# Kernel optimization log

Measured on AMD Instinct MI355X. Metric: run time of the kernel, lower is better.

## Reference

```python
import jax, jax.numpy as jnp
import numpy as np

EMBED_DIM = 768
NUM_HEADS = 12
HEAD_DIM = EMBED_DIM // NUM_HEADS
B, T = 2, 2048


def setup_inputs() -> dict:
    key = jax.random.key(0)
    ks = jax.random.split(key, 11)
    s = 1.0 / np.sqrt(EMBED_DIM)
    return {
        "query": jax.random.normal(ks[0], (B, T, EMBED_DIM), jnp.float32),
        "key_in": jax.random.normal(ks[1], (B, T, EMBED_DIM), jnp.float32),
        "value": jax.random.normal(ks[2], (B, T, EMBED_DIM), jnp.float32),
        "Wq": jax.random.uniform(ks[3], (EMBED_DIM, EMBED_DIM), jnp.float32, -s, s),
        "bq": jnp.zeros((EMBED_DIM,), jnp.float32),
        "Wk": jax.random.uniform(ks[4], (EMBED_DIM, EMBED_DIM), jnp.float32, -s, s),
        "bk": jnp.zeros((EMBED_DIM,), jnp.float32),
        "Wv": jax.random.uniform(ks[5], (EMBED_DIM, EMBED_DIM), jnp.float32, -s, s),
        "bv": jnp.zeros((EMBED_DIM,), jnp.float32),
        "Wo": jax.random.uniform(ks[6], (EMBED_DIM, EMBED_DIM), jnp.float32, -s, s),
        "bo": jnp.zeros((EMBED_DIM,), jnp.float32),
    }


def reference(query, key_in, value, Wq, bq, Wk, bk, Wv, bv, Wo, bo):
    b, t, _ = query.shape

    def split_heads(x):  # [B,T,E] -> [B,H,T,Dh]
        return x.reshape(b, t, NUM_HEADS, HEAD_DIM).transpose(0, 2, 1, 3)

    Q = split_heads(query @ Wq + bq)
    K = split_heads(key_in @ Wk + bk)
    V = split_heads(value @ Wv + bv)

    scores = jnp.einsum("bhqd,bhkd->bhqk", Q, K) / np.sqrt(HEAD_DIM).astype(np.float32)
    attn = jax.nn.softmax(scores, axis=-1)
    out = jnp.einsum("bhqk,bhkd->bhqd", attn, V)  # [B,H,T,Dh]
    out = out.transpose(0, 2, 1, 3).reshape(b, t, EMBED_DIM)
    return out @ Wo + bo
```

## Files before the change

kernel.cpp:

```cpp
#include <hip/hip_runtime.h>
#include <math.h>

typedef __attribute__((ext_vector_type(4))) float  floatx4;
typedef __attribute__((ext_vector_type(8))) short  short8;
typedef __attribute__((ext_vector_type(4))) short  short4v;
typedef __attribute__((ext_vector_type(8))) __bf16 bf16x8;

#define E_DIM 768
#define T_DIM 2048
#define N_B   2
#define N_H   12
#define H_D   64
#define M_TOT 4096

#define Q_SCALE 0.1803368801111204f

#if __has_builtin(__builtin_amdgcn_exp2f)
#define EXP2F(x) __builtin_amdgcn_exp2f(x)
#else
#define EXP2F(x) exp2f(x)
#endif
#if __has_builtin(__builtin_amdgcn_rcpf)
#define RCPF(x) __builtin_amdgcn_rcpf(x)
#else
#define RCPF(x) (1.0f / (x))
#endif

__device__ __forceinline__ unsigned short f32_to_bf16(float f) {
  unsigned int u = __float_as_uint(f);
  u += 0x7fffu + ((u >> 16) & 1u);
  return (unsigned short)(u >> 16);
}

__device__ __forceinline__ unsigned short f32_to_bf16_trunc(float f) {
  return (unsigned short)(__float_as_uint(f) >> 16);
}

__device__ __forceinline__ void gload_lds16(const unsigned short* g, unsigned short* l) {
  __builtin_amdgcn_global_load_lds(
      (const __attribute__((address_space(1))) unsigned int*)(const void*)g,
      (__attribute__((address_space(3))) unsigned int*)(void*)l, 16, 0, 0);
}

__global__ __launch_bounds__(256) void prep(const float* __restrict__ q,
                                            const float* __restrict__ k,
                                            const float* __restrict__ v,
                                            const float* __restrict__ W0,
                                            const float* __restrict__ W1,
                                            const float* __restrict__ W2,
                                            const float* __restrict__ W3,
                                            unsigned short* __restrict__ Xb,
                                            unsigned short* __restrict__ Wt) {
  __shared__ float tile[32][33];
  const int bx = blockIdx.x;
  if (bx < 9216) {
    const int z = bx / 3072, inner = bx % 3072;
    const float* src = (z == 0) ? q : (z == 1) ? k : v;
    size_t idx = ((size_t)inner * 256 + threadIdx.x) * 4;
    float4 val = *reinterpret_cast<const float4*>(&src[idx]);
    short4v o;
    o[0] = (short)f32_to_bf16(val.x);
    o[1] = (short)f32_to_bf16(val.y);
    o[2] = (short)f32_to_bf16(val.z);
    o[3] = (short)f32_to_bf16(val.w);
    *reinterpret_cast<short4v*>(&Xb[(size_t)z * M_TOT * E_DIM + idx]) = o;
  } else {
    const int t = bx - 9216;
    const int z = t / 576, rem = t % 576;
    const float* W = (z == 0) ? W0 : (z == 1) ? W1 : (z == 2) ? W2 : W3;
    unsigned short* dst = Wt + (size_t)z * E_DIM * E_DIM;
    int k0 = (rem / 24) * 32, n0 = (rem % 24) * 32;
    int tx = threadIdx.x & 31, ty = threadIdx.x >> 5;
    for (int i = 0; i < 4; i++)
      tile[ty + i * 8][tx] = W[(size_t)(k0 + ty + i * 8) * E_DIM + n0 + tx];
    __syncthreads();
    for (int i = 0; i < 4; i++)
      dst[(size_t)(n0 + ty + i * 8) * E_DIM + k0 + tx] = f32_to_bf16(tile[tx][ty + i * 8]);
  }
}

__global__ __launch_bounds__(256) void gemm_qkv(const unsigned short* __restrict__ Xb,
                                                const unsigned short* __restrict__ WtAll,
                                                const float* __restrict__ bq,
                                                const float* __restrict__ bk,
                                                const float* __restrict__ bv,
                                                unsigned short* __restrict__ outQKV,
                                                unsigned short* __restrict__ VTout) {
  __shared__ unsigned short As[128 * 32];
  __shared__ unsigned short Bs[128 * 32];

  const int z = blockIdx.z;
  const unsigned short* A = Xb + (size_t)z * M_TOT * E_DIM;
  const float* bias = (z == 0) ? bq : (z == 1) ? bk : bv;
  const unsigned short* W = WtAll + (size_t)z * E_DIM * E_DIM;
  unsigned short* out = outQKV + (size_t)z * M_TOT * E_DIM;
  const float scale = (z == 0) ? Q_SCALE : 1.0f;

  const int tid = threadIdx.x;
  const int lane = tid & 63, wv = tid >> 6;
  const int m15 = lane & 15, quad = lane >> 4;
  const int wm = (wv & 1) * 64, wn = (wv >> 1) * 64;
  const int m0 = blockIdx.x * 128, n0 = blockIdx.y * 128;

  floatx4 acc[4][4] = {};
  const int srow = lane >> 2, scol = (lane & 3) * 8;

  for (int k0 = 0; k0 < E_DIM; k0 += 32) {
    for (int cc = 0; cc < 2; cc++) {
      int c = wv * 2 + cc;
      gload_lds16(&A[(size_t)(m0 + c * 16 + srow) * E_DIM + k0 + scol], &As[c * 512]);
      gload_lds16(&W[(size_t)(n0 + c * 16 + srow) * E_DIM + k0 + scol], &Bs[c * 512]);
    }
    __syncthreads();
    bf16x8 af[4], bfr[4];
    for (int i = 0; i < 4; i++)
      af[i] = *reinterpret_cast<const bf16x8*>(&As[(wm + i * 16 + m15) * 32 + quad * 8]);
    for (int j = 0; j < 4; j++)
      bfr[j] = *reinterpret_cast<const bf16x8*>(&Bs[(wn + j * 16 + m15) * 32 + quad * 8]);
    for (int i = 0; i < 4; i++)
      for (int j = 0; j < 4; j++)
        acc[i][j] = __builtin_amdgcn_mfma_f32_16x16x32_bf16(af[i], bfr[j], acc[i][j], 0, 0, 0);
    __syncthreads();
  }

  if (z == 2) {
    for (int i = 0; i < 4; i++)
      for (int j = 0; j < 4; j++) {
        int gn = n0 + wn + j * 16 + m15;
        int hh = gn >> 6, d = gn & 63;
        float bso = bias[gn];
        int gm0 = m0 + wm + i * 16 + quad * 4;
        int bb2 = gm0 >> 11, t0 = gm0 & 2047;
        unsigned int d0 = ((unsigned int)f32_to_bf16(acc[i][j][1] + bso) << 16) |
                          f32_to_bf16(acc[i][j][0] + bso);
        unsigned int d1 = ((unsigned int)f32_to_bf16(acc[i][j][3] + bso) << 16) |
                          f32_to_bf16(acc[i][j][2] + bso);
        uint2 dd; dd.x = d0; dd.y = d1;
        *reinterpret_cast<uint2*>(
            &VTout[(((size_t)bb2 * N_H + hh) * H_D + d) * T_DIM + t0]) = dd;
      }
  } else {
    for (int i = 0; i < 4; i++)
      for (int j = 0; j < 4; j++) {
        int gn = n0 + wn + j * 16 + m15;
        int h = gn >> 6, d = gn & 63;
        float bso = bias[gn];
        for (int r = 0; r < 4; r++) {
          int gm = m0 + wm + i * 16 + quad * 4 + r;
          int bb = gm >> 11, tt = gm & 2047;
          float vv = (acc[i][j][r] + bso) * scale;
          out[(((size_t)bb * N_H + h) * T_DIM + tt) * H_D + d] = f32_to_bf16(vv);
        }
      }
  }
}

__global__ __launch_bounds__(256) void attn(const unsigned short* __restrict__ QKV,
                                            const unsigned short* __restrict__ VT,
                                            unsigned short* __restrict__ ctx) {
  __shared__ unsigned short Kbuf[2][2][64 * 64];
  __shared__ unsigned short strips[4][32 * 72];

  const int qb = blockIdx.x, h = blockIdx.y, bb = blockIdx.z;
  const size_t headoff = (((size_t)bb * N_H + h) * T_DIM) * H_D;
  const unsigned short* Qg = QKV + headoff;
  const unsigned short* Kg = QKV + (size_t)M_TOT * E_DIM + headoff;
  const unsigned short* VTg = VT + (((size_t)bb * N_H + h) * H_D) * T_DIM;

  const int tid = threadIdx.x, lane = tid & 63, wv = tid >> 6;
  const int m15 = lane & 15, quad = lane >> 4;
  const int qs = wv & 1, ks = wv >> 1;
  const int q0 = qb * 64 + qs * 32;

  auto stage = [&](int t0, int ping) {
#pragma unroll
    for (int i = 0; i < 4; i++) {
      int c = tid + i * 256;
      int tile = c >> 9, cc = c & 511;
      int key = cc >> 3, dc = cc & 7;
      int dcs = dc ^ (key & 7);
      gload_lds16(&Kg[((size_t)(t0 + tile) * 64 + key) * 64 + dcs * 8],
                  &Kbuf[ping][tile][cc * 8]);
    }
  };

  stage(0, 0);

  bf16x8 aq[2][2];
  for (int g = 0; g < 2; g++)
    for (int kk = 0; kk < 2; kk++)
      aq[g][kk] = __builtin_bit_cast(bf16x8, *reinterpret_cast<const short8*>(
          &Qg[(size_t)(q0 + g * 16 + m15) * 64 + kk * 32 + quad * 8]));

  const unsigned short* vbase = VTg + (size_t)(m15 * 2048 + quad * 8);
#define VFRAG(kt, nt, kk2) \
  (*reinterpret_cast<const short8*>(vbase + (size_t)(nt) * 32768 + (kt) * 64 + (kk2) * 32))

  short8 vf[8];
#pragma unroll
  for (int nt = 0; nt < 4; nt++)
    for (int kk2 = 0; kk2 < 2; kk2++) vf[nt * 2 + kk2] = VFRAG(ks, nt, kk2);

  floatx4 o[2][4] = {};
  floatx4 lacc[2] = {};
  const short8 ones_s = {0x3f80, 0x3f80, 0x3f80, 0x3f80, 0x3f80, 0x3f80, 0x3f80, 0x3f80};
  const bf16x8 onesb = __builtin_bit_cast(bf16x8, ones_s);
  unsigned short* strip = strips[wv];

  for (int r = 0; r < 16; r++) {
    __syncthreads();
    if (r < 15) stage(2 * r + 2, (r + 1) & 1);
    const unsigned short* Kt = Kbuf[r & 1][ks];
    const int kt = 2 * r + ks;

    floatx4 s[2][4] = {};
    for (int kk = 0; kk < 2; kk++)
#pragma unroll
      for (int mt = 0; mt < 4; mt++) {
        bf16x8 a = *reinterpret_cast<const bf16x8*>(
            &Kt[(mt * 16 + m15) * 64 + (((kk * 4 + quad) ^ (m15 & 7)) * 8)]);
        s[0][mt] = __builtin_amdgcn_mfma_f32_16x16x32_bf16(a, aq[0][kk], s[0][mt], 0, 0, 0);
        s[1][mt] = __builtin_amdgcn_mfma_f32_16x16x32_bf16(a, aq[1][kk], s[1][mt], 0, 0, 0);
      }

    for (int g = 0; g < 2; g++)
#pragma unroll
      for (int mt = 0; mt < 4; mt++) {
        unsigned int d0 = ((unsigned int)f32_to_bf16_trunc(EXP2F(s[g][mt][1])) << 16) |
                          f32_to_bf16_trunc(EXP2F(s[g][mt][0]));
        unsigned int d1 = ((unsigned int)f32_to_bf16_trunc(EXP2F(s[g][mt][3])) << 16) |
                          f32_to_bf16_trunc(EXP2F(s[g][mt][2]));
        uint2 dd; dd.x = d0; dd.y = d1;
        *reinterpret_cast<uint2*>(&strip[(g * 16 + m15) * 72 + mt * 16 + quad * 4]) = dd;
      }
    asm volatile("s_waitcnt lgkmcnt(0)" ::: "memory");

    for (int kk2 = 0; kk2 < 2; kk2++)
      for (int g = 0; g < 2; g++) {
        bf16x8 a = *reinterpret_cast<const bf16x8*>(
            &strip[(g * 16 + m15) * 72 + kk2 * 32 + quad * 8]);
        lacc[g] = __builtin_amdgcn_mfma_f32_16x16x32_bf16(a, onesb, lacc[g], 0, 0, 0);
#pragma unroll
        for (int nt = 0; nt < 4; nt++)
          o[g][nt] = __builtin_amdgcn_mfma_f32_16x16x32_bf16(
              a, __builtin_bit_cast(bf16x8, vf[nt * 2 + kk2]), o[g][nt], 0, 0, 0);
      }

    if (r < 15)
#pragma unroll
      for (int nt = 0; nt < 4; nt++)
        for (int kk2 = 0; kk2 < 2; kk2++) vf[nt * 2 + kk2] = VFRAG(kt + 2, nt, kk2);
  }
#undef VFRAG

  __syncthreads();
  float* red = (float*)&Kbuf[0][0][0];
  if (ks == 1) {
    floatx4* dst = (floatx4*)(red + (size_t)(qs * 64 + lane) * 40);
#pragma unroll
    for (int g = 0; g < 2; g++)
      for (int nt = 0; nt < 4; nt++) dst[g * 4 + nt] = o[g][nt];
    dst[8] = lacc[0];
    dst[9] = lacc[1];
  }
  __syncthreads();
  if (ks == 0) {
    const floatx4* src = (const floatx4*)(red + (size_t)(qs * 64 + lane) * 40);
#pragma unroll
    for (int g = 0; g < 2; g++)
      for (int nt = 0; nt < 4; nt++) o[g][nt] += src[g * 4 + nt];
    lacc[0] += src[8];
    lacc[1] += src[9];
    for (int g = 0; g < 2; g++)
      for (int r4 = 0; r4 < 4; r4++) {
        float rl = RCPF(lacc[g][r4]);
        int qq = q0 + g * 16 + quad * 4 + r4;
        for (int nt = 0; nt < 4; nt++)
          ctx[(size_t)(bb * T_DIM + qq) * E_DIM + h * 64 + nt * 16 + m15] =
              f32_to_bf16(o[g][nt][r4] * rl);
      }
  }
}

__global__ __launch_bounds__(256) void gemm_out(const unsigned short* __restrict__ Actx,
                                                const unsigned short* __restrict__ Wt,
                                                const float* __restrict__ bias,
                                                float* __restrict__ out) {
  __shared__ unsigned short As[64 * 32];
  __shared__ unsigned short Bs[128 * 32];

  const int tid = threadIdx.x;
  const int lane = tid & 63, wv = tid >> 6;
  const int m15 = lane & 15, quad = lane >> 4;
  const int wm = (wv & 1) * 32, wn = (wv >> 1) * 64;
  const int m0 = blockIdx.x * 64, n0 = blockIdx.y * 128;

  floatx4 acc[2][4] = {};
  const int srow = lane >> 2, scol = (lane & 3) * 8;

  for (int k0 = 0; k0 < E_DIM; k0 += 32) {
    gload_lds16(&Actx[(size_t)(m0 + wv * 16 + srow) * E_DIM + k0 + scol], &As[wv * 512]);
    for (int cc = 0; cc < 2; cc++) {
      int c = wv * 2 + cc;
      gload_lds16(&Wt[(size_t)(n0 + c * 16 + srow) * E_DIM + k0 + scol], &Bs[c * 512]);
    }
    __syncthreads();
    bf16x8 af[2], bfr[4];
    for (int i = 0; i < 2; i++)
      af[i] = *reinterpret_cast<const bf16x8*>(&As[(wm + i * 16 + m15) * 32 + quad * 8]);
    for (int j = 0; j < 4; j++)
      bfr[j] = *reinterpret_cast<const bf16x8*>(&Bs[(wn + j * 16 + m15) * 32 + quad * 8]);
    for (int i = 0; i < 2; i++)
      for (int j = 0; j < 4; j++)
        acc[i][j] = __builtin_amdgcn_mfma_f32_16x16x32_bf16(af[i], bfr[j], acc[i][j], 0, 0, 0);
    __syncthreads();
  }

  for (int i = 0; i < 2; i++)
    for (int j = 0; j < 4; j++) {
      int gn = n0 + wn + j * 16 + m15;
      float bso = bias[gn];
      for (int r = 0; r < 4; r++) {
        int gm = m0 + wm + i * 16 + quad * 4 + r;
        out[(size_t)gm * E_DIM + gn] = acc[i][j][r] + bso;
      }
    }
}

extern "C" void kernel_launch(void* const* d_in, const int* in_sizes, int n_in,
                              void* d_out, int out_size, void* d_ws, size_t ws_size,
                              hipStream_t stream) {
  const float* query  = (const float*)d_in[0];
  const float* key_in = (const float*)d_in[1];
  const float* value  = (const float*)d_in[2];
  const float* Wq = (const float*)d_in[3];
  const float* bq = (const float*)d_in[4];
  const float* Wk = (const float*)d_in[5];
  const float* bk = (const float*)d_in[6];
  const float* Wv = (const float*)d_in[7];
  const float* bv = (const float*)d_in[8];
  const float* Wo = (const float*)d_in[9];
  const float* bo = (const float*)d_in[10];
  float* out = (float*)d_out;

  unsigned short* ws  = (unsigned short*)d_ws;
  unsigned short* Wt  = ws;
  unsigned short* Xb  = Wt + (size_t)4 * E_DIM * E_DIM;
  unsigned short* QKV = Xb + (size_t)3 * M_TOT * E_DIM;
  unsigned short* VT  = QKV + (size_t)3 * M_TOT * E_DIM;
  unsigned short* ctx = VT + (size_t)N_B * N_H * H_D * T_DIM;

  dim3 tb(256);
  prep<<<dim3(11520), tb, 0, stream>>>(query, key_in, value, Wq, Wk, Wv, Wo, Xb, Wt);
  gemm_qkv<<<dim3(32, 6, 3), tb, 0, stream>>>(Xb, Wt, bq, bk, bv, QKV, VT);
  attn<<<dim3(32, 12, 2), tb, 0, stream>>>(QKV, VT, ctx);
  gemm_out<<<dim3(64, 6), tb, 0, stream>>>(ctx, Wt + (size_t)3 * E_DIM * E_DIM, bo, out);
  (void)in_sizes; (void)n_in; (void)out_size; (void)ws_size;
}
```

Baseline: 213.7 us.

## Software-pipeline attention with register K fragments and double-buffered P strips

The attention kernel stops staging K tiles through shared memory with block-wide barriers. Each wave now loads its K fragments straight from global memory into registers. The loop is skewed so that the PV MFMAs for the previous tile overlap the QK and exp work for the current tile, using double-buffered per-wave P strips. Launch bounds request 3 blocks per CU. The QKV GEMM also moves to a K-step of 64 with XOR-swizzled LDS, which halves the number of barrier pairs. The trade-offs are more register pressure and uncoalesced direct global loads of K.

```diff
diff --git a/kernel.cpp b/kernel.cpp
--- a/kernel.cpp
+++ b/kernel.cpp
@@ -86,8 +86,8 @@
                                                 const float* __restrict__ bv,
                                                 unsigned short* __restrict__ outQKV,
                                                 unsigned short* __restrict__ VTout) {
-  __shared__ unsigned short As[128 * 32];
-  __shared__ unsigned short Bs[128 * 32];
+  __shared__ unsigned short As[128 * 64];
+  __shared__ unsigned short Bs[128 * 64];
 
   const int z = blockIdx.z;
   const unsigned short* A = Xb + (size_t)z * M_TOT * E_DIM;
@@ -103,23 +103,31 @@
   const int m0 = blockIdx.x * 128, n0 = blockIdx.y * 128;
 
   floatx4 acc[4][4] = {};
-  const int srow = lane >> 2, scol = (lane & 3) * 8;
-
-  for (int k0 = 0; k0 < E_DIM; k0 += 32) {
-    for (int cc = 0; cc < 2; cc++) {
-      int c = wv * 2 + cc;
-      gload_lds16(&A[(size_t)(m0 + c * 16 + srow) * E_DIM + k0 + scol], &As[c * 512]);
-      gload_lds16(&W[(size_t)(n0 + c * 16 + srow) * E_DIM + k0 + scol], &Bs[c * 512]);
-    }
-    __syncthreads();
-    bf16x8 af[4], bfr[4];
-    for (int i = 0; i < 4; i++)
-      af[i] = *reinterpret_cast<const bf16x8*>(&As[(wm + i * 16 + m15) * 32 + quad * 8]);
-    for (int j = 0; j < 4; j++)
-      bfr[j] = *reinterpret_cast<const bf16x8*>(&Bs[(wn + j * 16 + m15) * 32 + quad * 8]);
-    for (int i = 0; i < 4; i++)
+  const int sw = m15 & 7;
+
+  for (int k0 = 0; k0 < E_DIM; k0 += 64) {
+#pragma unroll
+    for (int i = 0; i < 4; i++) {
+      int c = tid + i * 256;
+      int row = c >> 3, dc = c & 7;
+      int dcs = dc ^ (row & 7);
+      gload_lds16(&A[(size_t)(m0 + row) * E_DIM + k0 + dcs * 8], &As[c * 8]);
+      gload_lds16(&W[(size_t)(n0 + row) * E_DIM + k0 + dcs * 8], &Bs[c * 8]);
+    }
+    __syncthreads();
+#pragma unroll
+    for (int kk = 0; kk < 2; kk++) {
+      bf16x8 af[4], bfr[4];
+      for (int i = 0; i < 4; i++)
+        af[i] = *reinterpret_cast<const bf16x8*>(
+            &As[(wm + i * 16 + m15) * 64 + (((kk * 4 + quad) ^ sw) * 8)]);
       for (int j = 0; j < 4; j++)
-        acc[i][j] = __builtin_amdgcn_mfma_f32_16x16x32_bf16(af[i], bfr[j], acc[i][j], 0, 0, 0);
+        bfr[j] = *reinterpret_cast<const bf16x8*>(
+            &Bs[(wn + j * 16 + m15) * 64 + (((kk * 4 + quad) ^ sw) * 8)]);
+      for (int i = 0; i < 4; i++)
+        for (int j = 0; j < 4; j++)
+          acc[i][j] = __builtin_amdgcn_mfma_f32_16x16x32_bf16(af[i], bfr[j], acc[i][j], 0, 0, 0);
+    }
     __syncthreads();
   }
 
@@ -155,11 +163,10 @@
   }
 }
 
-__global__ __launch_bounds__(256) void attn(const unsigned short* __restrict__ QKV,
-                                            const unsigned short* __restrict__ VT,
-                                            unsigned short* __restrict__ ctx) {
-  __shared__ unsigned short Kbuf[2][2][64 * 64];
-  __shared__ unsigned short strips[4][32 * 72];
+__global__ __launch_bounds__(256, 3) void attn(const unsigned short* __restrict__ QKV,
+                                               const unsigned short* __restrict__ VT,
+                                               unsigned short* __restrict__ ctx) {
+  __shared__ unsigned short strips[4][2][32 * 72];
 
   const int qb = blockIdx.x, h = blockIdx.y, bb = blockIdx.z;
   const size_t headoff = (((size_t)bb * N_H + h) * T_DIM) * H_D;
@@ -172,19 +179,12 @@
   const int qs = wv & 1, ks = wv >> 1;
   const int q0 = qb * 64 + qs * 32;
 
-  auto stage = [&](int t0, int ping) {
-#pragma unroll
-    for (int i = 0; i < 4; i++) {
-      int c = tid + i * 256;
-      int tile = c >> 9, cc = c & 511;
-      int key = cc >> 3, dc = cc & 7;
-      int dcs = dc ^ (key & 7);
-      gload_lds16(&Kg[((size_t)(t0 + tile) * 64 + key) * 64 + dcs * 8],
-                  &Kbuf[ping][tile][cc * 8]);
-    }
-  };
-
-  stage(0, 0);
+  const unsigned short* kbase = Kg + (size_t)(m15 * 64 + quad * 8);
+  const unsigned short* vbase = VTg + (size_t)(m15 * 2048 + quad * 8);
+#define KFRAG(kt, mt, kk) \
+  (*reinterpret_cast<const short8*>(kbase + (size_t)(kt) * 4096 + (mt) * 1024 + (kk) * 32))
+#define VFRAG(kt, nt, kk2) \
+  (*reinterpret_cast<const short8*>(vbase + (size_t)(nt) * 32768 + (kt) * 64 + (kk2) * 32))
 
   bf16x8 aq[2][2];
   for (int g = 0; g < 2; g++)
@@ -192,69 +192,102 @@
       aq[g][kk] = __builtin_bit_cast(bf16x8, *reinterpret_cast<const short8*>(
           &Qg[(size_t)(q0 + g * 16 + m15) * 64 + kk * 32 + quad * 8]));
 
-  const unsigned short* vbase = VTg + (size_t)(m15 * 2048 + quad * 8);
-#define VFRAG(kt, nt, kk2) \
-  (*reinterpret_cast<const short8*>(vbase + (size_t)(nt) * 32768 + (kt) * 64 + (kk2) * 32))
-
-  short8 vf[8];
-#pragma unroll
-  for (int nt = 0; nt < 4; nt++)
-    for (int kk2 = 0; kk2 < 2; kk2++) vf[nt * 2 + kk2] = VFRAG(ks, nt, kk2);
+  short8 kf[8], vf[8];
+#pragma unroll
+  for (int mt = 0; mt < 4; mt++)
+    for (int kk = 0; kk < 2; kk++) {
+      kf[mt * 2 + kk] = KFRAG(ks, mt, kk);
+      vf[mt * 2 + kk] = VFRAG(ks, mt, kk);
+    }
 
   floatx4 o[2][4] = {};
   floatx4 lacc[2] = {};
   const short8 ones_s = {0x3f80, 0x3f80, 0x3f80, 0x3f80, 0x3f80, 0x3f80, 0x3f80, 0x3f80};
   const bf16x8 onesb = __builtin_bit_cast(bf16x8, ones_s);
-  unsigned short* strip = strips[wv];
-
-  for (int r = 0; r < 16; r++) {
-    __syncthreads();
-    if (r < 15) stage(2 * r + 2, (r + 1) & 1);
-    const unsigned short* Kt = Kbuf[r & 1][ks];
+
+  {
+    unsigned short* sp = strips[wv][0];
+    for (int g = 0; g < 2; g++) {
+      floatx4 s[4] = {};
+      for (int kk = 0; kk < 2; kk++)
+#pragma unroll
+        for (int mt = 0; mt < 4; mt++)
+          s[mt] = __builtin_amdgcn_mfma_f32_16x16x32_bf16(
+              __builtin_bit_cast(bf16x8, kf[mt * 2 + kk]), aq[g][kk], s[mt], 0, 0, 0);
+#pragma unroll
+      for (int mt = 0; mt < 4; mt++) {
+        unsigned int d0 = ((unsigned int)f32_to_bf16_trunc(EXP2F(s[mt][1])) << 16) |
+                          f32_to_bf16_trunc(EXP2F(s[mt][0]));
+        unsigned int d1 = ((unsigned int)f32_to_bf16_trunc(EXP2F(s[mt][3])) << 16) |
+                          f32_to_bf16_trunc(EXP2F(s[mt][2]));
+        uint2 dd; dd.x = d0; dd.y = d1;
+        *reinterpret_cast<uint2*>(&sp[(g * 16 + m15) * 72 + mt * 16 + quad * 4]) = dd;
+      }
+    }
+#pragma unroll
+    for (int mt = 0; mt < 4; mt++)
+      for (int kk = 0; kk < 2; kk++) kf[mt * 2 + kk] = KFRAG(ks + 2, mt, kk);
+    asm volatile("s_waitcnt lgkmcnt(0)" ::: "memory");
+  }
+
+  for (int r = 1; r < 16; r++) {
     const int kt = 2 * r + ks;
-
-    floatx4 s[2][4] = {};
-    for (int kk = 0; kk < 2; kk++)
-#pragma unroll
-      for (int mt = 0; mt < 4; mt++) {
-        bf16x8 a = *reinterpret_cast<const bf16x8*>(
-            &Kt[(mt * 16 + m15) * 64 + (((kk * 4 + quad) ^ (m15 & 7)) * 8)]);
-        s[0][mt] = __builtin_amdgcn_mfma_f32_16x16x32_bf16(a, aq[0][kk], s[0][mt], 0, 0, 0);
-        s[1][mt] = __builtin_amdgcn_mfma_f32_16x16x32_bf16(a, aq[1][kk], s[1][mt], 0, 0, 0);
-      }
-
-    for (int g = 0; g < 2; g++)
-#pragma unroll
-      for (int mt = 0; mt < 4; mt++) {
-        unsigned int d0 = ((unsigned int)f32_to_bf16_trunc(EXP2F(s[g][mt][1])) << 16) |
-                          f32_to_bf16_trunc(EXP2F(s[g][mt][0]));
-        unsigned int d1 = ((unsigned int)f32_to_bf16_trunc(EXP2F(s[g][mt][3])) << 16) |
-                          f32_to_bf16_trunc(EXP2F(s[g][mt][2]));
-        uint2 dd; dd.x = d0; dd.y = d1;
-        *reinterpret_cast<uint2*>(&strip[(g * 16 + m15) * 72 + mt * 16 + quad * 4]) = dd;
-      }
-    asm volatile("s_waitcnt lgkmcnt(0)" ::: "memory");
+    unsigned short* sp_prev = strips[wv][(r - 1) & 1];
+    unsigned short* sp_cur = strips[wv][r & 1];
 
     for (int kk2 = 0; kk2 < 2; kk2++)
       for (int g = 0; g < 2; g++) {
         bf16x8 a = *reinterpret_cast<const bf16x8*>(
-            &strip[(g * 16 + m15) * 72 + kk2 * 32 + quad * 8]);
+            &sp_prev[(g * 16 + m15) * 72 + kk2 * 32 + quad * 8]);
         lacc[g] = __builtin_amdgcn_mfma_f32_16x16x32_bf16(a, onesb, lacc[g], 0, 0, 0);
 #pragma unroll
         for (int nt = 0; nt < 4; nt++)
           o[g][nt] = __builtin_amdgcn_mfma_f32_16x16x32_bf16(
               a, __builtin_bit_cast(bf16x8, vf[nt * 2 + kk2]), o[g][nt], 0, 0, 0);
       }
-
+#pragma unroll
+    for (int nt = 0; nt < 4; nt++)
+      for (int kk2 = 0; kk2 < 2; kk2++) vf[nt * 2 + kk2] = VFRAG(kt, nt, kk2);
+
+    for (int g = 0; g < 2; g++) {
+      floatx4 s[4] = {};
+      for (int kk = 0; kk < 2; kk++)
+#pragma unroll
+        for (int mt = 0; mt < 4; mt++)
+          s[mt] = __builtin_amdgcn_mfma_f32_16x16x32_bf16(
+              __builtin_bit_cast(bf16x8, kf[mt * 2 + kk]), aq[g][kk], s[mt], 0, 0, 0);
+#pragma unroll
+      for (int mt = 0; mt < 4; mt++) {
+        unsigned int d0 = ((unsigned int)f32_to_bf16_trunc(EXP2F(s[mt][1])) << 16) |
+                          f32_to_bf16_trunc(EXP2F(s[mt][0]));
+        unsigned int d1 = ((unsigned int)f32_to_bf16_trunc(EXP2F(s[mt][3])) << 16) |
+                          f32_to_bf16_trunc(EXP2F(s[mt][2]));
+        uint2 dd; dd.x = d0; dd.y = d1;
+        *reinterpret_cast<uint2*>(&sp_cur[(g * 16 + m15) * 72 + mt * 16 + quad * 4]) = dd;
+      }
+    }
     if (r < 15)
 #pragma unroll
+      for (int mt = 0; mt < 4; mt++)
+        for (int kk = 0; kk < 2; kk++) kf[mt * 2 + kk] = KFRAG(kt + 2, mt, kk);
+    asm volatile("s_waitcnt lgkmcnt(0)" ::: "memory");
+  }
+
+  for (int kk2 = 0; kk2 < 2; kk2++)
+    for (int g = 0; g < 2; g++) {
+      bf16x8 a = *reinterpret_cast<const bf16x8*>(
+          &strips[wv][1][(g * 16 + m15) * 72 + kk2 * 32 + quad * 8]);
+      lacc[g] = __builtin_amdgcn_mfma_f32_16x16x32_bf16(a, onesb, lacc[g], 0, 0, 0);
+#pragma unroll
       for (int nt = 0; nt < 4; nt++)
-        for (int kk2 = 0; kk2 < 2; kk2++) vf[nt * 2 + kk2] = VFRAG(kt + 2, nt, kk2);
-  }
+        o[g][nt] = __builtin_amdgcn_mfma_f32_16x16x32_bf16(
+            a, __builtin_bit_cast(bf16x8, vf[nt * 2 + kk2]), o[g][nt], 0, 0, 0);
+    }
+#undef KFRAG
 #undef VFRAG
 
   __syncthreads();
-  float* red = (float*)&Kbuf[0][0][0];
+  float* red = (float*)&strips[0][0][0];
   if (ks == 1) {
     floatx4* dst = (floatx4*)(red + (size_t)(qs * 64 + lane) * 40);
 #pragma unroll
```

New measurement: 240.6 us. +12.6%, slower.
